# Kernel tuning notes

Hardware: AMD Instinct MI355X
Metric: run time of the kernel (lower is better)

The kernel has to match this reference:

```python
import jax, jax.numpy as jnp
import numpy as np

B, S, P, N = 256, 128, 100, 500
E, H, L, F = 256, 4, 2, 1024   # embed, heads, layers, ffn
V, U, I = 50000, 10000, 10000


def setup_inputs() -> dict:
    key = jax.random.key(0)
    ks = jax.random.split(key, 32)
    u = lambda k, shp: jax.random.uniform(k, shp, jnp.float32, -0.1, 0.1)
    n = lambda k, shp, s=0.02: jax.random.normal(k, shp, jnp.float32) * s
    inp = {
        'attr': jax.random.randint(ks[0], (B, S), 0, V),
        'attr_inds': jax.random.randint(ks[1], (B, S), 0, S),
        'attr_tf': jax.random.uniform(ks[2], (B, S), jnp.float32),
        'attr_feat': jax.random.normal(ks[3], (B, 13), jnp.float32),
        'attr_lens': jax.random.randint(ks[4], (B,), S // 2, S + 1).at[0].set(S),
        'attr_lens_user': jax.random.randint(ks[5], (B,), 0, S),
        'attr_lens_item': jax.random.randint(ks[6], (B,), 0, S),
        'user_ids': jax.random.randint(ks[7], (B,), 0, U),
        'item_ids': jax.random.randint(ks[8], (B,), 0, I),
        'pos_targets': jax.random.randint(ks[9], (B, P), 0, V),
        'pos_lens': jax.random.randint(ks[10], (B,), 1, P + 1).at[0].set(P),
        'neg_targets': jax.random.randint(ks[11], (B, N), 0, V),
        'neg_lens': jax.random.randint(ks[12], (B,), 1, N + 1).at[0].set(N),
        # parameters (init_uniform(-0.1,0.1) like f_init_weight)
        'attr_emb': u(ks[13], (V, E)),
        'user_emb': u(ks[14], (U, E)),
        'item_emb': u(ks[15], (I, E)),
        'out_emb': u(ks[16], (V, 3 * E)),
        'fw_W': n(ks[17], (1, 13), 0.1),
        'fw_b': jnp.zeros((1,), jnp.float32),
        'qkv_w': n(ks[18], (L, 3 * E, E)),
        'qkv_b': jnp.zeros((L, 3 * E), jnp.float32),
        'attn_out_w': n(ks[19], (L, E, E)),
        'attn_out_b': jnp.zeros((L, E), jnp.float32),
        'ln1_s': jnp.ones((L, E), jnp.float32),
        'ln1_b': jnp.zeros((L, E), jnp.float32),
        'ff1_w': n(ks[20], (L, F, E)),
        'ff1_b': jnp.zeros((L, F), jnp.float32),
        'ff2_w': n(ks[21], (L, E, F)),
        'ff2_b': jnp.zeros((L, E), jnp.float32),
        'ln2_s': jnp.ones((L, E), jnp.float32),
        'ln2_b': jnp.zeros((L, E), jnp.float32),
    }
    return inp


def _ln(x, s, b, eps=1e-5):
    m = jnp.mean(x, axis=-1, keepdims=True)
    v = jnp.mean(jnp.square(x - m), axis=-1, keepdims=True)
    return (x - m) * jax.lax.rsqrt(v + eps) * s + b


def _encoder_layer(x, pad, p):
    # PyTorch TransformerEncoderLayer (post-norm, relu, dropout=0/eval)
    b, s, e = x.shape
    hd = e // H
    qkv = x @ p['qkv_w'].T + p['qkv_b']                      # [B,S,3E]
    q, k, v = jnp.split(qkv, 3, axis=-1)
    q = q.reshape(b, s, H, hd)
    k = k.reshape(b, s, H, hd)
    v = v.reshape(b, s, H, hd)
    scores = jnp.einsum('bqhd,bkhd->bhqk', q, k) / jnp.sqrt(jnp.float32(hd))
    scores = scores + jnp.where(pad[:, None, None, :], -1e9, 0.0)
    a = jax.nn.softmax(scores, axis=-1)
    o = jnp.einsum('bhqk,bkhd->bqhd', a, v).reshape(b, s, e)
    o = o @ p['attn_out_w'].T + p['attn_out_b']
    x = _ln(x + o, p['ln1_s'], p['ln1_b'])
    h = jax.nn.relu(x @ p['ff1_w'].T + p['ff1_b'])
    h = h @ p['ff2_w'].T + p['ff2_b']
    return _ln(x + h, p['ln2_s'], p['ln2_b'])


def reference(attr, attr_inds, attr_tf, attr_feat, attr_lens, attr_lens_user,
              attr_lens_item, user_ids, item_ids, pos_targets, pos_lens,
              neg_targets, neg_lens, attr_emb, user_emb, item_emb, out_emb,
              fw_W, fw_b, qkv_w, qkv_b, attn_out_w, attn_out_b, ln1_s, ln1_b,
              ff1_w, ff1_b, ff2_w, ff2_b, ln2_s, ln2_b):
    b, s = attr.shape
    pos = jnp.arange(s)
    pad = pos[None, :] >= attr_lens[:, None]                 # True = padding
    x = attr_emb[attr]                                       # [B,S,E]
    for l in range(qkv_w.shape[0]):
        p = {'qkv_w': qkv_w[l], 'qkv_b': qkv_b[l],
             'attn_out_w': attn_out_w[l], 'attn_out_b': attn_out_b[l],
             'ln1_s': ln1_s[l], 'ln1_b': ln1_b[l],
             'ff1_w': ff1_w[l], 'ff1_b': ff1_b[l],
             'ff2_w': ff2_w[l], 'ff2_b': ff2_b[l],
             'ln2_s': ln2_s[l], 'ln2_b': ln2_b[l]}
        x = _encoder_layer(x, pad, p)
    # per-sample scalar user weight; vectorized ragged user/item tf weighting
    w_user = jax.nn.sigmoid(attr_feat @ fw_W.T + fw_b)[:, 0]           # [B]
    side = jnp.where(pos[None, :] < attr_lens_user[:, None],
                     w_user[:, None], 1.0 - w_user[:, None])           # [B,S]
    weight = attr_tf * side * (~pad)                                   # [B,S]
    attr_x = jnp.einsum('bs,bse->be', weight, x)                       # [B,E]
    output = jnp.concatenate([user_emb[user_ids], attr_x,
                              item_emb[item_ids]], axis=-1)            # [B,3E]
    pos_logits = jnp.einsum('bpe,be->bp', out_emb[pos_targets], output)
    neg_logits = jnp.einsum('bne,be->bn', out_emb[neg_targets], output)
    pos_valid = jnp.arange(pos_targets.shape[1])[None, :] < pos_lens[:, None]
    neg_valid = jnp.arange(neg_targets.shape[1])[None, :] < neg_lens[:, None]
    logits = jnp.concatenate([pos_logits, neg_logits], axis=-1)
    mask = jnp.concatenate([pos_valid, neg_valid], axis=-1)
    new_targets = jnp.concatenate([jnp.ones_like(pos_targets),
                                   jnp.zeros_like(neg_targets)], axis=1)
    new_targets = new_targets * mask.astype(new_targets.dtype)
    return logits, mask, new_targets
```

## Files before the change

kernel.cpp:

```cpp
#include <hip/hip_runtime.h>
#include <hip/hip_bf16.h>

typedef __bf16 bf16_t;
typedef __bf16 bf16x8 __attribute__((ext_vector_type(8)));
typedef __bf16 bf16x4 __attribute__((ext_vector_type(4)));
typedef float f32x4 __attribute__((ext_vector_type(4)));

#define B_ 256
#define S_ 128
#define E_ 256
#define H_ 4
#define HD_ 64
#define F_ 1024
#define TPOS_ 100
#define TNEG_ 500
#define TT_ 600
#define ROWS_ (B_ * S_)

__global__ void cvt_kernel(const float* __restrict__ in, bf16_t* __restrict__ out, int n) {
    int i = blockIdx.x * 256 + threadIdx.x;
    if (i < n) out[i] = (bf16_t)in[i];
}

__global__ __launch_bounds__(256) void embed_kernel(const int* __restrict__ attr,
        const float* __restrict__ emb, float* __restrict__ x, bf16_t* __restrict__ xb) {
    int row = blockIdx.x * 4 + (threadIdx.x >> 6);
    int lane = threadIdx.x & 63;
    int idx = attr[row];
    float4 v = reinterpret_cast<const float4*>(emb + (size_t)idx * E_)[lane];
    if (x) reinterpret_cast<float4*>(x + (size_t)row * E_)[lane] = v;
    bf16x4 o; o[0] = (bf16_t)v.x; o[1] = (bf16_t)v.y; o[2] = (bf16_t)v.z; o[3] = (bf16_t)v.w;
    *reinterpret_cast<bf16x4*>(xb + (size_t)row * E_ + lane * 4) = o;
}

template<bool RELU>
__global__ __launch_bounds__(256) void gemm_kernel(
        const bf16_t* __restrict__ A, const bf16_t* __restrict__ W,
        const float* __restrict__ bias, bf16_t* __restrict__ outB, int M, int N, int K) {
    __shared__ bf16_t lA[2][128 * 32];
    __shared__ bf16_t lB[2][128 * 32];
    int tid = threadIdx.x;
    int wave = tid >> 6, lane = tid & 63;
    int wr = wave >> 1, wc = wave & 1;
    int mBase = blockIdx.y * 128;
    int nBase = blockIdx.x * 128;
    int r16 = lane & 15, kg = lane >> 4;

    int srow = wave * 16 + (lane >> 2);
    int scol = (lane & 3) * 8;
    const bf16_t* gA = A + (size_t)(mBase + srow) * K + scol;
    const bf16_t* gB = W + (size_t)(nBase + srow) * K + scol;
    int ldst = wave * 512;

    f32x4 acc[4][4] = {};

    #define STAGE(buf, k0) { \
        _Pragma("unroll") \
        for (int iss = 0; iss < 2; iss++) { \
            __builtin_amdgcn_global_load_lds( \
                (const __attribute__((address_space(1))) void*)(gA + (size_t)iss * 64 * K + (k0)), \
                (__attribute__((address_space(3))) void*)(&lA[buf][iss * 2048 + ldst]), 16, 0, 0); \
            __builtin_amdgcn_global_load_lds( \
                (const __attribute__((address_space(1))) void*)(gB + (size_t)iss * 64 * K + (k0)), \
                (__attribute__((address_space(3))) void*)(&lB[buf][iss * 2048 + ldst]), 16, 0, 0); \
        } }

    STAGE(0, 0);
    int cur = 0;
    for (int k0 = 0; k0 < K; k0 += 32) {
        __syncthreads();
        if (k0 + 32 < K) STAGE(cur ^ 1, k0 + 32);
        bf16x8 a[4], b[4];
        #pragma unroll
        for (int i = 0; i < 4; i++) {
            a[i] = *reinterpret_cast<const bf16x8*>(&lA[cur][(wr * 64 + i * 16 + r16) * 32 + kg * 8]);
            b[i] = *reinterpret_cast<const bf16x8*>(&lB[cur][(wc * 64 + i * 16 + r16) * 32 + kg * 8]);
        }
        #pragma unroll
        for (int mi = 0; mi < 4; mi++)
            #pragma unroll
            for (int ni = 0; ni < 4; ni++)
                acc[mi][ni] = __builtin_amdgcn_mfma_f32_16x16x32_bf16(a[mi], b[ni], acc[mi][ni], 0, 0, 0);
        cur ^= 1;
    }
    #undef STAGE

    #pragma unroll
    for (int mi = 0; mi < 4; mi++) {
        #pragma unroll
        for (int ni = 0; ni < 4; ni++) {
            int col = nBase + wc * 64 + ni * 16 + r16;
            float bv = bias[col];
            #pragma unroll
            for (int j = 0; j < 4; j++) {
                int row = mBase + wr * 64 + mi * 16 + kg * 4 + j;
                float v = acc[mi][ni][j] + bv;
                if (RELU) v = v > 0.f ? v : 0.f;
                outB[(size_t)row * N + col] = (bf16_t)v;
            }
        }
    }
}

__global__ __launch_bounds__(256) void attn_kernel(const bf16_t* __restrict__ qkv,
        const int* __restrict__ lens, bf16_t* __restrict__ out) {
    __shared__ bf16_t p[S_][S_ + 8];
    __shared__ bf16_t vl[HD_][S_ + 8];
    int bh = blockIdx.x; int b = bh >> 2, h = bh & 3;
    int wave = threadIdx.x >> 6, lane = threadIdx.x & 63;
    int r16 = lane & 15, kg = lane >> 4;
    int q0 = wave * 32;
    int len = lens[b];
    const bf16_t* qbase = qkv + (size_t)b * S_ * 768;

    {
        int sl = (wave & 1) * 64 + lane;
        const bf16_t* vsrc = qbase + (size_t)sl * 768 + 512 + h * HD_;
        #pragma unroll
        for (int pass = 0; pass < 4; pass++) {
            int d0 = (pass * 2 + (wave >> 1)) * 8;
            bf16x8 v = *reinterpret_cast<const bf16x8*>(vsrc + d0);
            #pragma unroll
            for (int j = 0; j < 8; j++) vl[d0 + j][sl] = v[j];
        }
    }

    f32x4 acc[2][8] = {};
    #pragma unroll
    for (int ks = 0; ks < 2; ks++) {
        int kOff = h * HD_ + ks * 32 + kg * 8;
        bf16x8 a[2], bb[8];
        #pragma unroll
        for (int mi = 0; mi < 2; mi++)
            a[mi] = *reinterpret_cast<const bf16x8*>(qbase + (size_t)(q0 + mi * 16 + r16) * 768 + kOff);
        #pragma unroll
        for (int ni = 0; ni < 8; ni++)
            bb[ni] = *reinterpret_cast<const bf16x8*>(qbase + (size_t)(ni * 16 + r16) * 768 + 256 + kOff);
        #pragma unroll
        for (int mi = 0; mi < 2; mi++)
            #pragma unroll
            for (int ni = 0; ni < 8; ni++)
                acc[mi][ni] = __builtin_amdgcn_mfma_f32_16x16x32_bf16(a[mi], bb[ni], acc[mi][ni], 0, 0, 0);
    }
    #pragma unroll
    for (int mi = 0; mi < 2; mi++) {
        #pragma unroll
        for (int j = 0; j < 4; j++) {
            float vals[8]; float mx = -1e30f;
            #pragma unroll
            for (int ni = 0; ni < 8; ni++) {
                int kp = ni * 16 + r16;
                float v = acc[mi][ni][j] * 0.125f;
                vals[ni] = (kp < len) ? v : -1e30f;
                mx = fmaxf(mx, vals[ni]);
            }
            #pragma unroll
            for (int m = 1; m < 16; m <<= 1) mx = fmaxf(mx, __shfl_xor(mx, m));
            float sum = 0.f;
            #pragma unroll
            for (int ni = 0; ni < 8; ni++) {
                vals[ni] = (vals[ni] > -1e29f) ? __expf(vals[ni] - mx) : 0.f;
                sum += vals[ni];
            }
            #pragma unroll
            for (int m = 1; m < 16; m <<= 1) sum += __shfl_xor(sum, m);
            float inv = 1.0f / sum;
            int row = q0 + mi * 16 + kg * 4 + j;
            #pragma unroll
            for (int ni = 0; ni < 8; ni++)
                p[row][ni * 16 + r16] = (bf16_t)(vals[ni] * inv);
        }
    }
    __syncthreads();
    f32x4 acc2[2][4] = {};
    #pragma unroll
    for (int ks = 0; ks < 4; ks++) {
        int k = ks * 32 + kg * 8;
        bf16x8 a[2], bb[4];
        #pragma unroll
        for (int mi = 0; mi < 2; mi++)
            a[mi] = *reinterpret_cast<const bf16x8*>(&p[q0 + mi * 16 + r16][k]);
        #pragma unroll
        for (int ni = 0; ni < 4; ni++)
            bb[ni] = *reinterpret_cast<const bf16x8*>(&vl[ni * 16 + r16][k]);
        #pragma unroll
        for (int mi = 0; mi < 2; mi++)
            #pragma unroll
            for (int ni = 0; ni < 4; ni++)
                acc2[mi][ni] = __builtin_amdgcn_mfma_f32_16x16x32_bf16(a[mi], bb[ni], acc2[mi][ni], 0, 0, 0);
    }
    #pragma unroll
    for (int mi = 0; mi < 2; mi++)
        #pragma unroll
        for (int ni = 0; ni < 4; ni++)
            #pragma unroll
            for (int j = 0; j < 4; j++) {
                int q = q0 + mi * 16 + kg * 4 + j;
                int d = ni * 16 + r16;
                out[((size_t)b * S_ + q) * E_ + h * HD_ + d] = (bf16_t)acc2[mi][ni][j];
            }
}

__global__ __launch_bounds__(256) void ln_kernel(const bf16_t* __restrict__ xin,
        const bf16_t* __restrict__ res, const float* __restrict__ sc, const float* __restrict__ bi,
        float* __restrict__ xout, bf16_t* __restrict__ xbout) {
    int row = blockIdx.x * 4 + (threadIdx.x >> 6);
    int lane = threadIdx.x & 63;
    bf16x4 a = *reinterpret_cast<const bf16x4*>(xin + (size_t)row * E_ + lane * 4);
    bf16x4 r = *reinterpret_cast<const bf16x4*>(res + (size_t)row * E_ + lane * 4);
    float v0 = (float)a[0] + (float)r[0];
    float v1 = (float)a[1] + (float)r[1];
    float v2 = (float)a[2] + (float)r[2];
    float v3 = (float)a[3] + (float)r[3];
    float s = v0 + v1 + v2 + v3;
    #pragma unroll
    for (int m = 1; m < 64; m <<= 1) s += __shfl_xor(s, m);
    float mean = s * (1.0f / E_);
    float d0 = v0 - mean, d1 = v1 - mean, d2 = v2 - mean, d3 = v3 - mean;
    float vs = d0 * d0 + d1 * d1 + d2 * d2 + d3 * d3;
    #pragma unroll
    for (int m = 1; m < 64; m <<= 1) vs += __shfl_xor(vs, m);
    float inv = rsqrtf(vs * (1.0f / E_) + 1e-5f);
    float4 scv = reinterpret_cast<const float4*>(sc)[lane];
    float4 biv = reinterpret_cast<const float4*>(bi)[lane];
    float o0 = d0 * inv * scv.x + biv.x, o1 = d1 * inv * scv.y + biv.y;
    float o2 = d2 * inv * scv.z + biv.z, o3 = d3 * inv * scv.w + biv.w;
    if (xout) {
        float4 o; o.x = o0; o.y = o1; o.z = o2; o.w = o3;
        reinterpret_cast<float4*>(xout + (size_t)row * E_)[lane] = o;
    }
    bf16x4 ov; ov[0] = (bf16_t)o0; ov[1] = (bf16_t)o1; ov[2] = (bf16_t)o2; ov[3] = (bf16_t)o3;
    *reinterpret_cast<bf16x4*>(xbout + (size_t)row * E_ + lane * 4) = ov;
}

__global__ void wuser_kernel(const float* __restrict__ feat, const float* __restrict__ W,
                             const float* __restrict__ bb, float* __restrict__ wu) {
    int b = threadIdx.x;
    if (b < B_) {
        float z = bb[0];
        #pragma unroll
        for (int i = 0; i < 13; i++) z += feat[b * 13 + i] * W[i];
        wu[b] = 1.f / (1.f + __expf(-z));
    }
}

template<bool USEX>
__global__ __launch_bounds__(256) void pool_kernel(
        const float* __restrict__ x, const bf16_t* __restrict__ xb,
        const float* __restrict__ attr_tf,
        const int* __restrict__ lens, const int* __restrict__ lens_user,
        const float* __restrict__ wu, const int* __restrict__ uid, const int* __restrict__ iid,
        const float* __restrict__ user_emb, const float* __restrict__ item_emb,
        float* __restrict__ outvec) {
    int b = blockIdx.x, t = threadIdx.x;
    __shared__ float wrow[S_];
    if (t < S_) {
        float w = (t < lens[b]) ? attr_tf[b * S_ + t] : 0.f;
        float side = (t < lens_user[b]) ? wu[b] : (1.f - wu[b]);
        wrow[t] = w * side;
    }
    __syncthreads();
    float acc = 0.f;
    if (USEX) {
        const float* xr = x + (size_t)b * S_ * E_ + t;
        #pragma unroll 4
        for (int s = 0; s < S_; s++) acc += wrow[s] * xr[(size_t)s * E_];
    } else {
        const bf16_t* xr = xb + (size_t)b * S_ * E_ + t;
        #pragma unroll 4
        for (int s = 0; s < S_; s++) acc += wrow[s] * (float)xr[(size_t)s * E_];
    }
    outvec[b * 768 + 256 + t] = acc;
    outvec[b * 768 + t] = user_emb[(size_t)uid[b] * E_ + t];
    outvec[b * 768 + 512 + t] = item_emb[(size_t)iid[b] * E_ + t];
}

__global__ __launch_bounds__(256) void logits_kernel(
        const float* __restrict__ outvec, const float* __restrict__ out_emb,
        const int* __restrict__ pos_t, const int* __restrict__ pos_l,
        const int* __restrict__ neg_t, const int* __restrict__ neg_l,
        float* __restrict__ dout) {
    int g = blockIdx.x * 4 + (threadIdx.x >> 6);
    int lane = threadIdx.x & 63;
    int b = g / TT_, t = g - b * TT_;
    int tgt, valid, ispos;
    if (t < TPOS_) { tgt = pos_t[b * TPOS_ + t]; valid = (t < pos_l[b]); ispos = 1; }
    else { int tn = t - TPOS_; tgt = neg_t[b * TNEG_ + tn]; valid = (tn < neg_l[b]); ispos = 0; }
    const float4* e4 = reinterpret_cast<const float4*>(out_emb + (size_t)tgt * 768);
    const float4* o4 = reinterpret_cast<const float4*>(outvec + (size_t)b * 768);
    float acc = 0.f;
    #pragma unroll
    for (int c = 0; c < 3; c++) {
        float4 a = e4[c * 64 + lane];
        float4 o = o4[c * 64 + lane];
        acc += a.x * o.x + a.y * o.y + a.z * o.z + a.w * o.w;
    }
    #pragma unroll
    for (int m = 1; m < 64; m <<= 1) acc += __shfl_xor(acc, m);
    if (lane == 0) {
        size_t i = (size_t)b * TT_ + t;
        dout[i] = acc;
        dout[(size_t)B_ * TT_ + i] = valid ? 1.0f : 0.0f;
        dout[2 * (size_t)B_ * TT_ + i] = (valid && ispos) ? 1.0f : 0.0f;
    }
}

extern "C" void kernel_launch(void* const* d_in, const int* in_sizes, int n_in,
                              void* d_out, int out_size, void* d_ws, size_t ws_size,
                              hipStream_t stream) {
    const int*   attr        = (const int*)d_in[0];
    const float* attr_tf     = (const float*)d_in[2];
    const float* attr_feat   = (const float*)d_in[3];
    const int*   attr_lens   = (const int*)d_in[4];
    const int*   attr_lens_u = (const int*)d_in[5];
    const int*   user_ids    = (const int*)d_in[7];
    const int*   item_ids    = (const int*)d_in[8];
    const int*   pos_targets = (const int*)d_in[9];
    const int*   pos_lens    = (const int*)d_in[10];
    const int*   neg_targets = (const int*)d_in[11];
    const int*   neg_lens    = (const int*)d_in[12];
    const float* attr_emb    = (const float*)d_in[13];
    const float* user_emb    = (const float*)d_in[14];
    const float* item_emb    = (const float*)d_in[15];
    const float* out_emb     = (const float*)d_in[16];
    const float* fw_W        = (const float*)d_in[17];
    const float* fw_b        = (const float*)d_in[18];
    const float* qkv_w       = (const float*)d_in[19];
    const float* qkv_b       = (const float*)d_in[20];
    const float* attn_out_w  = (const float*)d_in[21];
    const float* attn_out_b  = (const float*)d_in[22];
    const float* ln1_s       = (const float*)d_in[23];
    const float* ln1_b       = (const float*)d_in[24];
    const float* ff1_w       = (const float*)d_in[25];
    const float* ff1_b       = (const float*)d_in[26];
    const float* ff2_w       = (const float*)d_in[27];
    const float* ff2_b       = (const float*)d_in[28];
    const float* ln2_s       = (const float*)d_in[29];
    const float* ln2_b       = (const float*)d_in[30];

    size_t szRes = (size_t)ROWS_ * E_ * 2;
    size_t wElems = (size_t)2 * 768 * 256 + (size_t)2 * 256 * 256
                  + (size_t)2 * 1024 * 256 + (size_t)2 * 256 * 1024;
    size_t fixedB = 3 * szRes + wElems * 2 + (size_t)B_ * 768 * 4 + 4096 + 16384;
    size_t szX = (size_t)ROWS_ * E_ * 4;
    int CH = -1; bool useX = false;
    for (int pass = 0; pass < 2 && CH < 0; ++pass) {
        bool ux = (pass == 0);
        for (int ch = 1; ch <= 32; ch <<= 1) {
            size_t need = fixedB + (ux ? szX : 0) + (size_t)(ROWS_ / ch) * 1024 * 2;
            if (need <= ws_size) { CH = ch; useX = ux; break; }
        }
    }
    if (CH < 0) { CH = 32; useX = false; }
    int rowsC = ROWS_ / CH, sampC = B_ / CH;

    char* ws = (char*)d_ws;
    size_t off = 0;
    auto alloc = [&](size_t bytes) { void* pp = ws + off; off += (bytes + 255) & ~255ULL; return pp; };
    bf16_t* xb  = (bf16_t*)alloc(szRes);
    bf16_t* ob  = (bf16_t*)alloc(szRes);
    bf16_t* g   = (bf16_t*)alloc(szRes);
    bf16_t* wq  = (bf16_t*)alloc((size_t)2 * 768 * 256 * 2);
    bf16_t* wa  = (bf16_t*)alloc((size_t)2 * 256 * 256 * 2);
    bf16_t* w1  = (bf16_t*)alloc((size_t)2 * 1024 * 256 * 2);
    bf16_t* w2  = (bf16_t*)alloc((size_t)2 * 256 * 1024 * 2);
    float* outvec = (float*)alloc((size_t)B_ * 768 * 4);
    float* wu     = (float*)alloc(1024);
    float* x      = useX ? (float*)alloc(szX) : nullptr;
    bf16_t* chunk = (bf16_t*)alloc((size_t)rowsC * 1024 * 2);

    cvt_kernel<<<(2 * 768 * 256 + 255) / 256, 256, 0, stream>>>(qkv_w, wq, 2 * 768 * 256);
    cvt_kernel<<<(2 * 256 * 256 + 255) / 256, 256, 0, stream>>>(attn_out_w, wa, 2 * 256 * 256);
    cvt_kernel<<<(2 * 1024 * 256 + 255) / 256, 256, 0, stream>>>(ff1_w, w1, 2 * 1024 * 256);
    cvt_kernel<<<(2 * 256 * 1024 + 255) / 256, 256, 0, stream>>>(ff2_w, w2, 2 * 256 * 1024);

    embed_kernel<<<ROWS_ / 4, 256, 0, stream>>>(attr, attr_emb, x, xb);

    for (int l = 0; l < 2; l++) {
        for (int c = 0; c < CH; c++) {
            size_t r0 = (size_t)c * rowsC;
            gemm_kernel<false><<<dim3(6, rowsC / 128), 256, 0, stream>>>(
                xb + r0 * E_, wq + (size_t)l * 768 * 256, qkv_b + l * 768, chunk, rowsC, 768, 256);
            attn_kernel<<<sampC * H_, 256, 0, stream>>>(chunk, attr_lens + c * sampC, ob + r0 * E_);
        }
        gemm_kernel<false><<<dim3(2, 256), 256, 0, stream>>>(
            ob, wa + (size_t)l * 256 * 256, attn_out_b + l * 256, g, ROWS_, 256, 256);
        ln_kernel<<<ROWS_ / 4, 256, 0, stream>>>(xb, g, ln1_s + l * 256, ln1_b + l * 256, x, xb);
        for (int c = 0; c < CH; c++) {
            size_t r0 = (size_t)c * rowsC;
            gemm_kernel<true><<<dim3(8, rowsC / 128), 256, 0, stream>>>(
                xb + r0 * E_, w1 + (size_t)l * 1024 * 256, ff1_b + l * 1024, chunk, rowsC, 1024, 256);
            gemm_kernel<false><<<dim3(2, rowsC / 128), 256, 0, stream>>>(
                chunk, w2 + (size_t)l * 256 * 1024, ff2_b + l * 256, g + r0 * E_, rowsC, 256, 1024);
        }
        ln_kernel<<<ROWS_ / 4, 256, 0, stream>>>(xb, g, ln2_s + l * 256, ln2_b + l * 256, x, xb);
    }

    wuser_kernel<<<1, 256, 0, stream>>>(attr_feat, fw_W, fw_b, wu);
    if (useX)
        pool_kernel<true><<<B_, 256, 0, stream>>>(x, xb, attr_tf, attr_lens, attr_lens_u, wu,
                                                  user_ids, item_ids, user_emb, item_emb, outvec);
    else
        pool_kernel<false><<<B_, 256, 0, stream>>>(x, xb, attr_tf, attr_lens, attr_lens_u, wu,
                                                   user_ids, item_ids, user_emb, item_emb, outvec);
    logits_kernel<<<B_ * TT_ / 4, 256, 0, stream>>>(outvec, out_emb, pos_targets, pos_lens,
                                                    neg_targets, neg_lens, (float*)d_out);
}
```

Measured before the change: 450.1 us.

## Fuse residual add and LayerNorm into full-row GEMM epilogue, drop fp32 residual

Adds a GEMM kernel whose 64-row tile spans all 256 output columns, so the attention-out and FFN2 projections can add bias and residual and apply LayerNorm in the epilogue. Each result is written in place to the bf16 residual buffer. This removes the separate LN kernels, the intermediate g buffer, and the fp32 copy of x. The four weight-conversion launches are merged into one. Risks: in-place read and write of xb within a block, variance computed as E[x^2]-mean^2, pooling now reads bf16 activations instead of fp32, and the wider tile lowers block count and occupancy.

```diff
diff --git a/kernel.cpp b/kernel.cpp
--- a/kernel.cpp
+++ b/kernel.cpp
@@ -17,18 +17,24 @@
 #define TT_ 600
 #define ROWS_ (B_ * S_)
 
-__global__ void cvt_kernel(const float* __restrict__ in, bf16_t* __restrict__ out, int n) {
+__global__ __launch_bounds__(256) void cvtall_kernel(
+        const float* __restrict__ sq, const float* __restrict__ sa,
+        const float* __restrict__ s1, const float* __restrict__ s2,
+        bf16_t* __restrict__ dq, bf16_t* __restrict__ da,
+        bf16_t* __restrict__ d1, bf16_t* __restrict__ d2) {
     int i = blockIdx.x * 256 + threadIdx.x;
-    if (i < n) out[i] = (bf16_t)in[i];
+    if (i < 393216) { dq[i] = (bf16_t)sq[i]; }
+    else if (i < 524288) { int j = i - 393216; da[j] = (bf16_t)sa[j]; }
+    else if (i < 1048576) { int j = i - 524288; d1[j] = (bf16_t)s1[j]; }
+    else { int j = i - 1048576; d2[j] = (bf16_t)s2[j]; }
 }
 
 __global__ __launch_bounds__(256) void embed_kernel(const int* __restrict__ attr,
-        const float* __restrict__ emb, float* __restrict__ x, bf16_t* __restrict__ xb) {
+        const float* __restrict__ emb, bf16_t* __restrict__ xb) {
     int row = blockIdx.x * 4 + (threadIdx.x >> 6);
     int lane = threadIdx.x & 63;
     int idx = attr[row];
     float4 v = reinterpret_cast<const float4*>(emb + (size_t)idx * E_)[lane];
-    if (x) reinterpret_cast<float4*>(x + (size_t)row * E_)[lane] = v;
     bf16x4 o; o[0] = (bf16_t)v.x; o[1] = (bf16_t)v.y; o[2] = (bf16_t)v.z; o[3] = (bf16_t)v.w;
     *reinterpret_cast<bf16x4*>(xb + (size_t)row * E_ + lane * 4) = o;
 }
@@ -102,6 +108,101 @@
     }
 }
 
+__global__ __launch_bounds__(256) void gemm_ln_kernel(
+        const bf16_t* __restrict__ A, const bf16_t* __restrict__ W,
+        const float* __restrict__ bias, const float* __restrict__ sc,
+        const float* __restrict__ bi, bf16_t* __restrict__ xb, int M, int K) {
+    __shared__ bf16_t lA[2][64 * 32];
+    __shared__ bf16_t lB[2][256 * 32];
+    __shared__ float psum[64][2][2];
+    int tid = threadIdx.x;
+    int wave = tid >> 6, lane = tid & 63;
+    int wm = wave >> 1, wn = wave & 1;
+    int mBase = blockIdx.x * 64;
+    int r16 = lane & 15, kg = lane >> 4;
+
+    const bf16_t* gA = A + (size_t)(mBase + wave * 16 + (lane >> 2)) * K + (lane & 3) * 8;
+    const bf16_t* gB = W + (size_t)((lane >> 2)) * K + (lane & 3) * 8;
+
+    f32x4 acc[2][8] = {};
+
+    #define STAGE2(buf, k0) { \
+        __builtin_amdgcn_global_load_lds( \
+            (const __attribute__((address_space(1))) void*)(gA + (k0)), \
+            (__attribute__((address_space(3))) void*)(&lA[buf][wave * 512]), 16, 0, 0); \
+        _Pragma("unroll") \
+        for (int iss = 0; iss < 4; iss++) { \
+            int q = wave * 4 + iss; \
+            __builtin_amdgcn_global_load_lds( \
+                (const __attribute__((address_space(1))) void*)(gB + (size_t)q * 16 * K + (k0)), \
+                (__attribute__((address_space(3))) void*)(&lB[buf][q * 512]), 16, 0, 0); \
+        } }
+
+    STAGE2(0, 0);
+    int cur = 0;
+    for (int k0 = 0; k0 < K; k0 += 32) {
+        __syncthreads();
+        if (k0 + 32 < K) STAGE2(cur ^ 1, k0 + 32);
+        bf16x8 a[2], b[8];
+        #pragma unroll
+        for (int mi = 0; mi < 2; mi++)
+            a[mi] = *reinterpret_cast<const bf16x8*>(&lA[cur][(wm * 32 + mi * 16 + r16) * 32 + kg * 8]);
+        #pragma unroll
+        for (int ni = 0; ni < 8; ni++)
+            b[ni] = *reinterpret_cast<const bf16x8*>(&lB[cur][(wn * 128 + ni * 16 + r16) * 32 + kg * 8]);
+        #pragma unroll
+        for (int mi = 0; mi < 2; mi++)
+            #pragma unroll
+            for (int ni = 0; ni < 8; ni++)
+                acc[mi][ni] = __builtin_amdgcn_mfma_f32_16x16x32_bf16(a[mi], b[ni], acc[mi][ni], 0, 0, 0);
+        cur ^= 1;
+    }
+    #undef STAGE2
+
+    float bv[8];
+    #pragma unroll
+    for (int ni = 0; ni < 8; ni++) bv[ni] = bias[wn * 128 + ni * 16 + r16];
+    #pragma unroll
+    for (int mi = 0; mi < 2; mi++) {
+        #pragma unroll
+        for (int j = 0; j < 4; j++) {
+            int rl = wm * 32 + mi * 16 + kg * 4 + j;
+            const bf16_t* rrow = xb + (size_t)(mBase + rl) * 256;
+            float s = 0.f, q = 0.f;
+            #pragma unroll
+            for (int ni = 0; ni < 8; ni++) {
+                int col = wn * 128 + ni * 16 + r16;
+                float v = acc[mi][ni][j] + bv[ni] + (float)rrow[col];
+                acc[mi][ni][j] = v;
+                s += v; q += v * v;
+            }
+            #pragma unroll
+            for (int m = 1; m < 16; m <<= 1) { s += __shfl_xor(s, m); q += __shfl_xor(q, m); }
+            if (r16 == 0) { psum[rl][wn][0] = s; psum[rl][wn][1] = q; }
+        }
+    }
+    __syncthreads();
+    #pragma unroll
+    for (int mi = 0; mi < 2; mi++) {
+        #pragma unroll
+        for (int j = 0; j < 4; j++) {
+            int rl = wm * 32 + mi * 16 + kg * 4 + j;
+            float s = psum[rl][0][0] + psum[rl][1][0];
+            float qq = psum[rl][0][1] + psum[rl][1][1];
+            float mean = s * (1.0f / 256.0f);
+            float var = qq * (1.0f / 256.0f) - mean * mean;
+            float inv = rsqrtf(var + 1e-5f);
+            bf16_t* orow = xb + (size_t)(mBase + rl) * 256;
+            #pragma unroll
+            for (int ni = 0; ni < 8; ni++) {
+                int col = wn * 128 + ni * 16 + r16;
+                float o = (acc[mi][ni][j] - mean) * inv * sc[col] + bi[col];
+                orow[col] = (bf16_t)o;
+            }
+        }
+    }
+}
+
 __global__ __launch_bounds__(256) void attn_kernel(const bf16_t* __restrict__ qkv,
         const int* __restrict__ lens, bf16_t* __restrict__ out) {
     __shared__ bf16_t p[S_][S_ + 8];
@@ -201,38 +302,6 @@
             }
 }
 
-__global__ __launch_bounds__(256) void ln_kernel(const bf16_t* __restrict__ xin,
-        const bf16_t* __restrict__ res, const float* __restrict__ sc, const float* __restrict__ bi,
-        float* __restrict__ xout, bf16_t* __restrict__ xbout) {
-    int row = blockIdx.x * 4 + (threadIdx.x >> 6);
-    int lane = threadIdx.x & 63;
-    bf16x4 a = *reinterpret_cast<const bf16x4*>(xin + (size_t)row * E_ + lane * 4);
-    bf16x4 r = *reinterpret_cast<const bf16x4*>(res + (size_t)row * E_ + lane * 4);
-    float v0 = (float)a[0] + (float)r[0];
-    float v1 = (float)a[1] + (float)r[1];
-    float v2 = (float)a[2] + (float)r[2];
-    float v3 = (float)a[3] + (float)r[3];
-    float s = v0 + v1 + v2 + v3;
-    #pragma unroll
-    for (int m = 1; m < 64; m <<= 1) s += __shfl_xor(s, m);
-    float mean = s * (1.0f / E_);
-    float d0 = v0 - mean, d1 = v1 - mean, d2 = v2 - mean, d3 = v3 - mean;
-    float vs = d0 * d0 + d1 * d1 + d2 * d2 + d3 * d3;
-    #pragma unroll
-    for (int m = 1; m < 64; m <<= 1) vs += __shfl_xor(vs, m);
-    float inv = rsqrtf(vs * (1.0f / E_) + 1e-5f);
-    float4 scv = reinterpret_cast<const float4*>(sc)[lane];
-    float4 biv = reinterpret_cast<const float4*>(bi)[lane];
-    float o0 = d0 * inv * scv.x + biv.x, o1 = d1 * inv * scv.y + biv.y;
-    float o2 = d2 * inv * scv.z + biv.z, o3 = d3 * inv * scv.w + biv.w;
-    if (xout) {
-        float4 o; o.x = o0; o.y = o1; o.z = o2; o.w = o3;
-        reinterpret_cast<float4*>(xout + (size_t)row * E_)[lane] = o;
-    }
-    bf16x4 ov; ov[0] = (bf16_t)o0; ov[1] = (bf16_t)o1; ov[2] = (bf16_t)o2; ov[3] = (bf16_t)o3;
-    *reinterpret_cast<bf16x4*>(xbout + (size_t)row * E_ + lane * 4) = ov;
-}
-
 __global__ void wuser_kernel(const float* __restrict__ feat, const float* __restrict__ W,
                              const float* __restrict__ bb, float* __restrict__ wu) {
     int b = threadIdx.x;
@@ -244,10 +313,8 @@
     }
 }
 
-template<bool USEX>
 __global__ __launch_bounds__(256) void pool_kernel(
-        const float* __restrict__ x, const bf16_t* __restrict__ xb,
-        const float* __restrict__ attr_tf,
+        const bf16_t* __restrict__ xb, const float* __restrict__ attr_tf,
         const int* __restrict__ lens, const int* __restrict__ lens_user,
         const float* __restrict__ wu, const int* __restrict__ uid, const int* __restrict__ iid,
         const float* __restrict__ user_emb, const float* __restrict__ item_emb,
@@ -261,15 +328,9 @@
     }
     __syncthreads();
     float acc = 0.f;
-    if (USEX) {
-        const float* xr = x + (size_t)b * S_ * E_ + t;
-        #pragma unroll 4
-        for (int s = 0; s < S_; s++) acc += wrow[s] * xr[(size_t)s * E_];
-    } else {
-        const bf16_t* xr = xb + (size_t)b * S_ * E_ + t;
-        #pragma unroll 4
-        for (int s = 0; s < S_; s++) acc += wrow[s] * (float)xr[(size_t)s * E_];
-    }
+    const bf16_t* xr = xb + (size_t)b * S_ * E_ + t;
+    #pragma unroll 4
+    for (int s = 0; s < S_; s++) acc += wrow[s] * (float)xr[(size_t)s * E_];
     outvec[b * 768 + 256 + t] = acc;
     outvec[b * 768 + t] = user_emb[(size_t)uid[b] * E_ + t];
     outvec[b * 768 + 512 + t] = item_emb[(size_t)iid[b] * E_ + t];
@@ -339,19 +400,12 @@
     const float* ln2_b       = (const float*)d_in[30];
 
     size_t szRes = (size_t)ROWS_ * E_ * 2;
-    size_t wElems = (size_t)2 * 768 * 256 + (size_t)2 * 256 * 256
-                  + (size_t)2 * 1024 * 256 + (size_t)2 * 256 * 1024;
-    size_t fixedB = 3 * szRes + wElems * 2 + (size_t)B_ * 768 * 4 + 4096 + 16384;
-    size_t szX = (size_t)ROWS_ * E_ * 4;
-    int CH = -1; bool useX = false;
-    for (int pass = 0; pass < 2 && CH < 0; ++pass) {
-        bool ux = (pass == 0);
-        for (int ch = 1; ch <= 32; ch <<= 1) {
-            size_t need = fixedB + (ux ? szX : 0) + (size_t)(ROWS_ / ch) * 1024 * 2;
-            if (need <= ws_size) { CH = ch; useX = ux; break; }
-        }
-    }
-    if (CH < 0) { CH = 32; useX = false; }
+    size_t wB = (size_t)1572864 * 2;
+    size_t fixedB = 2 * szRes + wB + (size_t)B_ * 768 * 4 + 4096 + 16384;
+    int CH = 32;
+    for (int ch = 1; ch <= 32; ch <<= 1) {
+        if (fixedB + (size_t)(ROWS_ / ch) * 1024 * 2 <= ws_size) { CH = ch; break; }
+    }
     int rowsC = ROWS_ / CH, sampC = B_ / CH;
 
     char* ws = (char*)d_ws;
@@ -359,22 +413,16 @@
     auto alloc = [&](size_t bytes) { void* pp = ws + off; off += (bytes + 255) & ~255ULL; return pp; };
     bf16_t* xb  = (bf16_t*)alloc(szRes);
     bf16_t* ob  = (bf16_t*)alloc(szRes);
-    bf16_t* g   = (bf16_t*)alloc(szRes);
-    bf16_t* wq  = (bf16_t*)alloc((size_t)2 * 768 * 256 * 2);
-    bf16_t* wa  = (bf16_t*)alloc((size_t)2 * 256 * 256 * 2);
-    bf16_t* w1  = (bf16_t*)alloc((size_t)2 * 1024 * 256 * 2);
-    bf16_t* w2  = (bf16_t*)alloc((size_t)2 * 256 * 1024 * 2);
+    bf16_t* wq  = (bf16_t*)alloc((size_t)393216 * 2);
+    bf16_t* wa  = (bf16_t*)alloc((size_t)131072 * 2);
+    bf16_t* w1  = (bf16_t*)alloc((size_t)524288 * 2);
+    bf16_t* w2  = (bf16_t*)alloc((size_t)524288 * 2);
     float* outvec = (float*)alloc((size_t)B_ * 768 * 4);
     float* wu     = (float*)alloc(1024);
-    float* x      = useX ? (float*)alloc(szX) : nullptr;
     bf16_t* chunk = (bf16_t*)alloc((size_t)rowsC * 1024 * 2);
 
-    cvt_kernel<<<(2 * 768 * 256 + 255) / 256, 256, 0, stream>>>(qkv_w, wq, 2 * 768 * 256);
-    cvt_kernel<<<(2 * 256 * 256 + 255) / 256, 256, 0, stream>>>(attn_out_w, wa, 2 * 256 * 256);
-    cvt_kernel<<<(2 * 1024 * 256 + 255) / 256, 256, 0, stream>>>(ff1_w, w1, 2 * 1024 * 256);
-    cvt_kernel<<<(2 * 256 * 1024 + 255) / 256, 256, 0, stream>>>(ff2_w, w2, 2 * 256 * 1024);
-
-    embed_kernel<<<ROWS_ / 4, 256, 0, stream>>>(attr, attr_emb, x, xb);
+    cvtall_kernel<<<6144, 256, 0, stream>>>(qkv_w, attn_out_w, ff1_w, ff2_w, wq, wa, w1, w2);
+    embed_kernel<<<ROWS_ / 4, 256, 0, stream>>>(attr, attr_emb, xb);
 
     for (int l = 0; l < 2; l++) {
         for (int c = 0; c < CH; c++) {
@@ -383,26 +431,22 @@
                 xb + r0 * E_, wq + (size_t)l * 768 * 256, qkv_b + l * 768, chunk, rowsC, 768, 256);
             attn_kernel<<<sampC * H_, 256, 0, stream>>>(chunk, attr_lens + c * sampC, ob + r0 * E_);
         }
-        gemm_kernel<false><<<dim3(2, 256), 256, 0, stream>>>(
-            ob, wa + (size_t)l * 256 * 256, attn_out_b + l * 256, g, ROWS_, 256, 256);
-        ln_kernel<<<ROWS_ / 4, 256, 0, stream>>>(xb, g, ln1_s + l * 256, ln1_b + l * 256, x, xb);
+        gemm_ln_kernel<<<ROWS_ / 64, 256, 0, stream>>>(
+            ob, wa + (size_t)l * 256 * 256, attn_out_b + l * 256,
+            ln1_s + l * 256, ln1_b + l * 256, xb, ROWS_, 256);
         for (int c = 0; c < CH; c++) {
             size_t r0 = (size_t)c * rowsC;
             gemm_kernel<true><<<dim3(8, rowsC / 128), 256, 0, stream>>>(
                 xb + r0 * E_, w1 + (size_t)l * 1024 * 256, ff1_b + l * 1024, chunk, rowsC, 1024, 256);
-            gemm_kernel<false><<<dim3(2, rowsC / 128), 256, 0, stream>>>(
-                chunk, w2 + (size_t)l * 256 * 1024, ff2_b + l * 256, g + r0 * E_, rowsC, 256, 1024);
-        }
-        ln_kernel<<<ROWS_ / 4, 256, 0, stream>>>(xb, g, ln2_s + l * 256, ln2_b + l * 256, x, xb);
+            gemm_ln_kernel<<<rowsC / 64, 256, 0, stream>>>(
+                chunk, w2 + (size_t)l * 256 * 1024, ff2_b + l * 256,
+                ln2_s + l * 256, ln2_b + l * 256, xb + r0 * E_, rowsC, 1024);
+        }
     }
 
     wuser_kernel<<<1, 256, 0, stream>>>(attr_feat, fw_W, fw_b, wu);
-    if (useX)
-        pool_kernel<true><<<B_, 256, 0, stream>>>(x, xb, attr_tf, attr_lens, attr_lens_u, wu,
-                                                  user_ids, item_ids, user_emb, item_emb, outvec);
-    else
-        pool_kernel<false><<<B_, 256, 0, stream>>>(x, xb, attr_tf, attr_lens, attr_lens_u, wu,
-                                                   user_ids, item_ids, user_emb, item_emb, outvec);
+    pool_kernel<<<B_, 256, 0, stream>>>(xb, attr_tf, attr_lens, attr_lens_u, wu,
+                                        user_ids, item_ids, user_emb, item_emb, outvec);
     logits_kernel<<<B_ * TT_ / 4, 256, 0, stream>>>(outvec, out_emb, pos_targets, pos_lens,
                                                     neg_targets, neg_lens, (float*)d_out);
 }
```

After: 389.4 us. -13.5%, faster.
